# Kernel optimization log

Measured on AMD Instinct MI355X. Metric: run time of the kernel, lower is better.

## Reference

```python
import jax, jax.numpy as jnp
import numpy as np

ALPHA = 0.2  # LeakyReLU negative slope
N_NODES = 100000
N_EDGES = 3200000
IN_F = 256
OUT_F = 64

def setup_inputs() -> dict:
    key = jax.random.key(0)
    k1, k2, k3, k4 = jax.random.split(key, 4)
    inp = jax.random.uniform(k1, (N_NODES, IN_F), dtype=jnp.float32)
    edge = jax.random.randint(k2, (2, N_EDGES), 0, N_NODES, dtype=jnp.int64)
    # xavier_normal with gain=1.414
    g = 1.414
    W = jax.random.normal(k3, (IN_F, OUT_F), dtype=jnp.float32) * (g * np.sqrt(2.0 / (IN_F + OUT_F)))
    a = jax.random.normal(k4, (1, 2 * OUT_F), dtype=jnp.float32) * (g * np.sqrt(2.0 / (1 + 2 * OUT_F)))
    return {"input": inp, "edge": edge, "W": W, "a": a}

def reference(input, edge, W, a):
    N = input.shape[0]
    src, dst = edge[0], edge[1]
    h = input @ W                                  # [N, F]
    # a @ [h[src]; h[dst]] decomposed into per-node dot products
    a_src = a[0, :OUT_F]
    a_dst = a[0, OUT_F:]
    s_src = h @ a_src                              # [N]
    s_dst = h @ a_dst                              # [N]
    score = s_src[src] + s_dst[dst]                # [E]
    edge_e = jnp.exp(-jax.nn.leaky_relu(score, negative_slope=ALPHA))
    # e_rowsum = spmm(edge, edge_e, ones(N,1)) -> segment sum of edge_e over src rows
    e_rowsum = jax.ops.segment_sum(edge_e, src, num_segments=N)        # [N]
    # h_prime = spmm(edge, edge_e, h): row i = sum_e edge_e * h[dst]
    h_prime = jax.ops.segment_sum(edge_e[:, None] * h[dst], src, num_segments=N)  # [N, F]
    h_prime = h_prime / e_rowsum[:, None]
    return jax.nn.elu(h_prime)  # concat=True
```

## Files before the change

kernel.cpp:

```cpp
#include <hip/hip_runtime.h>
#include <hip/hip_bf16.h>
#include <math.h>

#define N_NODES 100000
#define N_EDGES 3200000
#define IN_F 256
#define OUT_F 64
#define LRELU_SLOPE 0.2f

#define NB 1563
#define CAP 3072

#define NBLK2 784
#define EPB 4096
#define XG 98
#define NE (NBLK2 * NB)
#define NS1 ((NE + 255) / 256)
#define S2PER ((NS1 + 255) / 256)

typedef __attribute__((ext_vector_type(8))) short bf16x8;
typedef __attribute__((ext_vector_type(4))) float f32x4;

__global__ __launch_bounds__(256) void wt_kernel(
    const float* __restrict__ W, __hip_bfloat16* __restrict__ wt) {
  wt[blockIdx.x * 256 + threadIdx.x] =
      __float2bfloat16(W[threadIdx.x * 64 + blockIdx.x]);
}

__global__ __launch_bounds__(256) void gemm_h_kernel(
    const float* __restrict__ in, const __hip_bfloat16* __restrict__ wt,
    const float* __restrict__ a, __hip_bfloat16* __restrict__ h,
    float* __restrict__ s_src, float* __restrict__ s_dst) {
  const int tid = threadIdx.x;
  const int w = tid >> 6, lane = tid & 63;
  const int lm = lane & 15, lg = lane >> 4;
  const int arow = blockIdx.x * 64 + w * 16 + lm;
  const bool rv = arow < N_NODES;
  const float* xrow = &in[(size_t)(rv ? arow : 0) * IN_F + lg * 8];

  f32x4 acc[4];
#pragma unroll
  for (int ct = 0; ct < 4; ++ct) acc[ct] = (f32x4){0.f, 0.f, 0.f, 0.f};

  const __hip_bfloat16* wbase = &wt[(size_t)lm * IN_F + lg * 8];

#pragma unroll
  for (int kt = 0; kt < 8; ++kt) {
    float4 xa = make_float4(0.f, 0.f, 0.f, 0.f);
    float4 xb = make_float4(0.f, 0.f, 0.f, 0.f);
    if (rv) {
      xa = *(const float4*)(xrow + kt * 32);
      xb = *(const float4*)(xrow + kt * 32 + 4);
    }
    union { __hip_bfloat16 s[8]; bf16x8 v; } u;
    u.s[0] = __float2bfloat16(xa.x); u.s[1] = __float2bfloat16(xa.y);
    u.s[2] = __float2bfloat16(xa.z); u.s[3] = __float2bfloat16(xa.w);
    u.s[4] = __float2bfloat16(xb.x); u.s[5] = __float2bfloat16(xb.y);
    u.s[6] = __float2bfloat16(xb.z); u.s[7] = __float2bfloat16(xb.w);
    const bf16x8 af = u.v;
#pragma unroll
    for (int ct = 0; ct < 4; ++ct) {
      bf16x8 bfr = *(const bf16x8*)(wbase + (size_t)ct * 16 * IN_F + kt * 32);
      acc[ct] = __builtin_amdgcn_mfma_f32_16x16x32_bf16(af, bfr, acc[ct],
                                                        0, 0, 0);
    }
  }

  float as[4], ad[4];
#pragma unroll
  for (int ct = 0; ct < 4; ++ct) {
    as[ct] = a[ct * 16 + lm];
    ad[ct] = a[OUT_F + ct * 16 + lm];
  }
#pragma unroll
  for (int reg = 0; reg < 4; ++reg) {
    const int row = blockIdx.x * 64 + w * 16 + lg * 4 + reg;
    float vs = 0.f, vd = 0.f;
    if (row < N_NODES) {
#pragma unroll
      for (int ct = 0; ct < 4; ++ct) {
        const float v = acc[ct][reg];
        h[(size_t)row * OUT_F + ct * 16 + lm] = __float2bfloat16(v);
        vs += v * as[ct];
        vd += v * ad[ct];
      }
    }
#pragma unroll
    for (int m = 1; m < 16; m <<= 1) {
      vs += __shfl_xor(vs, m);
      vd += __shfl_xor(vd, m);
    }
    if (lm == 0 && row < N_NODES) {
      s_src[row] = vs;
      s_dst[row] = vd;
    }
  }
}

__global__ __launch_bounds__(256) void hist2d_kernel(
    const int4* __restrict__ src4, int* __restrict__ cnt2d) {
  __shared__ int lh[NB];
  const int tid = threadIdx.x, b = blockIdx.x;
  for (int j = tid; j < NB; j += 256) lh[j] = 0;
  __syncthreads();
#pragma unroll
  for (int i = 0; i < 4; ++i) {
    const int idx4 = b * (EPB / 4) + i * 256 + tid;
    if (idx4 < N_EDGES / 4) {
      const int4 s = src4[idx4];
      atomicAdd(&lh[s.x >> 6], 1);
      atomicAdd(&lh[s.y >> 6], 1);
      atomicAdd(&lh[s.z >> 6], 1);
      atomicAdd(&lh[s.w >> 6], 1);
    }
  }
  __syncthreads();
  for (int j = tid; j < NB; j += 256) cnt2d[b * NB + j] = lh[j];
}

__device__ __forceinline__ int cnt2d_addr(int o) {
  const int j = o / NBLK2;
  const int rk = o - j * NBLK2;
  const int r = rk / XG;
  const int q = rk - r * XG;
  return (q * 8 + r) * NB + j;
}

__global__ __launch_bounds__(256) void scan1_kernel(
    int* __restrict__ cnt2d, int* __restrict__ pt) {
  __shared__ int ws[4];
  const int tid = threadIdx.x, lane = tid & 63, wv = tid >> 6;
  const int o = blockIdx.x * 256 + tid;
  int addr = 0, v = 0;
  if (o < NE) { addr = cnt2d_addr(o); v = cnt2d[addr]; }
  int incl = v;
#pragma unroll
  for (int off = 1; off < 64; off <<= 1) {
    const int t = __shfl_up(incl, off);
    if (lane >= off) incl += t;
  }
  if (lane == 63) ws[wv] = incl;
  __syncthreads();
  int base = 0;
#pragma unroll
  for (int k = 0; k < 4; ++k)
    if (k < wv) base += ws[k];
  if (o < NE) cnt2d[addr] = base + incl - v;
  if (tid == 255) pt[blockIdx.x] = base + incl;
}

__global__ __launch_bounds__(256) void scan2_kernel(int* __restrict__ pt) {
  __shared__ int ts[256];
  const int t = threadIdx.x;
  int local[S2PER];
  int sum = 0;
#pragma unroll
  for (int k = 0; k < S2PER; ++k) {
    const int o = t * S2PER + k;
    const int v = (o < NS1) ? pt[o] : 0;
    local[k] = sum;
    sum += v;
  }
  ts[t] = sum;
  __syncthreads();
  for (int off = 1; off < 256; off <<= 1) {
    int tv = (t >= off) ? ts[t - off] : 0;
    __syncthreads();
    ts[t] += tv;
    __syncthreads();
  }
  const int ex = (t > 0) ? ts[t - 1] : 0;
#pragma unroll
  for (int k = 0; k < S2PER; ++k) {
    const int o = t * S2PER + k;
    if (o < NS1) pt[o] = ex + local[k];
  }
}

__global__ __launch_bounds__(256) void scan3_kernel(
    int* __restrict__ cnt2d, const int* __restrict__ pt,
    int* __restrict__ bstart) {
  const int o = blockIdx.x * 256 + threadIdx.x;
  if (o < NE) {
    const int addr = cnt2d_addr(o);
    const int excl = cnt2d[addr] + pt[blockIdx.x];
    cnt2d[addr] = excl;
    const int j = o / NBLK2;
    if (o - j * NBLK2 == 0) bstart[j] = excl;
  }
  if (o == 0) bstart[NB] = N_EDGES;
}

__global__ __launch_bounds__(256) void scatter2_kernel(
    const int4* __restrict__ src4, const int4* __restrict__ dst4,
    const int* __restrict__ cnt2d, unsigned int* __restrict__ staged) {
  __shared__ int base[NB];
  const int tid = threadIdx.x, b = blockIdx.x;
  for (int j = tid; j < NB; j += 256) base[j] = cnt2d[b * NB + j];
  __syncthreads();
#pragma unroll
  for (int i = 0; i < 4; ++i) {
    const int idx4 = b * (EPB / 4) + i * 256 + tid;
    if (idx4 < N_EDGES / 4) {
      const int4 s = src4[idx4];
      const int4 d = dst4[idx4];
      int p;
      p = atomicAdd(&base[s.x >> 6], 1);
      staged[p] = ((unsigned)(s.x & 63) << 17) | (unsigned)d.x;
      p = atomicAdd(&base[s.y >> 6], 1);
      staged[p] = ((unsigned)(s.y & 63) << 17) | (unsigned)d.y;
      p = atomicAdd(&base[s.z >> 6], 1);
      staged[p] = ((unsigned)(s.z & 63) << 17) | (unsigned)d.z;
      p = atomicAdd(&base[s.w >> 6], 1);
      staged[p] = ((unsigned)(s.w & 63) << 17) | (unsigned)d.w;
    }
  }
}

__global__ __launch_bounds__(256) void sort_aggregate_kernel(
    const int* __restrict__ bstart, const unsigned int* __restrict__ staged,
    const float* __restrict__ s_src, const float* __restrict__ s_dst,
    const __hip_bfloat16* __restrict__ h, float* __restrict__ out) {
  __shared__ uint2 eds[CAP];
  __shared__ float ssrc[64];
  __shared__ int lcnt[64];
  __shared__ int lstart[65];
  __shared__ int lcur[64];

  const int b = blockIdx.x;
  const int tid = threadIdx.x;
  const int lane = tid & 63;
  const int wv = tid >> 6;
  const int node0 = b << 6;

  if (tid < 64)
    ssrc[tid] = (node0 + tid < N_NODES) ? s_src[node0 + tid] : 0.f;

  const int e0 = bstart[b];
  const int e1 = bstart[b + 1];

  float acc[16], rsn[16];
#pragma unroll
  for (int j = 0; j < 16; ++j) { acc[j] = 0.f; rsn[j] = 0.f; }

  for (int c0 = e0; c0 < e1; c0 += CAP) {
    const int cc = min(CAP, e1 - c0);
    __syncthreads();
    if (tid < 64) lcnt[tid] = 0;
    __syncthreads();

    for (int i = tid; i < cc; i += 256)
      atomicAdd(&lcnt[staged[c0 + i] >> 17], 1);
    __syncthreads();

    if (tid < 64) {
      int v = lcnt[tid];
#pragma unroll
      for (int off = 1; off < 64; off <<= 1) {
        int tv = __shfl_up(v, off);
        if (lane >= off) v += tv;
      }
      lstart[tid + 1] = v;
      if (tid == 0) lstart[0] = 0;
      lcur[tid] = v - lcnt[tid];
    }
    __syncthreads();

    for (int i = tid; i < cc; i += 256) {
      const unsigned pk = staged[c0 + i];
      const int ls = (int)(pk >> 17);
      const int d = (int)(pk & 0x1FFFFu);
      const float sc = ssrc[ls] + s_dst[d];
      const float lr = sc > 0.f ? sc : LRELU_SLOPE * sc;
      const float ev = __expf(-lr);
      const int p = atomicAdd(&lcur[ls], 1);
      eds[p] = make_uint2((unsigned)d, __float_as_uint(ev));
    }
    __syncthreads();

#pragma unroll
    for (int j = 0; j < 16; ++j) {
      const int n = wv + 4 * j;
      const int iend = lstart[n + 1];
      int i = lstart[n];
      float p0 = 0.f, p1 = 0.f, rv = 0.f;
      for (; i + 4 <= iend; i += 4) {
        const uint2 q0 = eds[i + 0], q1 = eds[i + 1];
        const uint2 q2 = eds[i + 2], q3 = eds[i + 3];
        const float v0 = __uint_as_float(q0.y), v1 = __uint_as_float(q1.y);
        const float v2 = __uint_as_float(q2.y), v3 = __uint_as_float(q3.y);
        const float h0 = __bfloat162float(h[(size_t)q0.x * OUT_F + lane]);
        const float h1 = __bfloat162float(h[(size_t)q1.x * OUT_F + lane]);
        const float h2 = __bfloat162float(h[(size_t)q2.x * OUT_F + lane]);
        const float h3 = __bfloat162float(h[(size_t)q3.x * OUT_F + lane]);
        p0 += v0 * h0 + v2 * h2;
        p1 += v1 * h1 + v3 * h3;
        rv += (v0 + v1) + (v2 + v3);
      }
      for (; i < iend; ++i) {
        const uint2 q0 = eds[i];
        const float v0 = __uint_as_float(q0.y);
        p0 += v0 * __bfloat162float(h[(size_t)q0.x * OUT_F + lane]);
        rv += v0;
      }
      acc[j] += p0 + p1;
      rsn[j] += rv;
    }
  }

#pragma unroll
  for (int j = 0; j < 16; ++j) {
    const int node = node0 + wv + 4 * j;
    if (node < N_NODES) {
      const float v = acc[j] / rsn[j];
      out[(size_t)node * OUT_F + lane] = v > 0.f ? v : expm1f(v);
    }
  }
}

extern "C" void kernel_launch(void* const* d_in, const int* in_sizes, int n_in,
                              void* d_out, int out_size, void* d_ws, size_t ws_size,
                              hipStream_t stream) {
  const float* in = (const float*)d_in[0];
  const int* edge = (const int*)d_in[1];
  const float* W = (const float*)d_in[2];
  const float* a = (const float*)d_in[3];
  float* out = (float*)d_out;

  const int4* src4 = (const int4*)edge;
  const int4* dst4 = (const int4*)(edge + N_EDGES);

  char* p = (char*)d_ws;
  __hip_bfloat16* h = (__hip_bfloat16*)p;  p += (size_t)N_NODES * OUT_F * 2;
  float* s_src = (float*)p;                p += (size_t)N_NODES * 4;
  float* s_dst = (float*)p;                p += (size_t)N_NODES * 4;
  unsigned int* staged = (unsigned int*)p; p += (size_t)N_EDGES * 4;
  int* bctr = (int*)p;                     p += (size_t)(NB * 32) * 4;
  int* bstart = (int*)p;                   p += (size_t)(NB + 1) * 4 + 12;
  __hip_bfloat16* wt = (__hip_bfloat16*)p; p += (size_t)OUT_F * IN_F * 2;
  (void)bctr;

  int* cnt2d = (int*)d_out;
  int* pt = (int*)((char*)d_out + (size_t)8 * 1024 * 1024);

  wt_kernel<<<OUT_F, 256, 0, stream>>>(W, wt);
  gemm_h_kernel<<<(N_NODES + 63) / 64, 256, 0, stream>>>(in, wt, a, h, s_src,
                                                         s_dst);
  hist2d_kernel<<<NBLK2, 256, 0, stream>>>(src4, cnt2d);
  scan1_kernel<<<NS1, 256, 0, stream>>>(cnt2d, pt);
  scan2_kernel<<<1, 256, 0, stream>>>(pt);
  scan3_kernel<<<NS1, 256, 0, stream>>>(cnt2d, pt, bstart);
  scatter2_kernel<<<NBLK2, 256, 0, stream>>>(src4, dst4, cnt2d, staged);
  sort_aggregate_kernel<<<NB, 256, 0, stream>>>(bstart, staged, s_src, s_dst,
                                                h, out);
}
```

Before: 416.5 us.

## Reduce bucket-sort partition blocks and use bucket-major count layout for scans

Shrinks the histogram/scatter grid from 784 to 256 blocks of 512 threads, so each block covers a larger edge chunk. The per-block count matrix becomes bucket-major with a block rank interleaved across XCD groups, so the scan reads and writes contiguously and each scan block maps exactly to one bucket. That removes the index arithmetic in the scans and lets the second-level scan write bucket starts directly. The count matrix shrinks, which cuts scan traffic, but fewer blocks means less parallelism in the atomic-heavy histogram and scatter passes.

```diff
diff --git a/kernel.cpp b/kernel.cpp
--- a/kernel.cpp
+++ b/kernel.cpp
@@ -11,12 +11,11 @@
 #define NB 1563
 #define CAP 3072
 
-#define NBLK2 784
-#define EPB 4096
-#define XG 98
-#define NE (NBLK2 * NB)
-#define NS1 ((NE + 255) / 256)
-#define S2PER ((NS1 + 255) / 256)
+#define NBLK2 256
+#define XG 32
+#define I4PB (N_EDGES / 4 / NBLK2)
+#define NE (NB * NBLK2)
+#define S2PER ((NB + 255) / 256)
 
 typedef __attribute__((ext_vector_type(8))) short bf16x8;
 typedef __attribute__((ext_vector_type(4))) float f32x4;
@@ -97,17 +96,19 @@
   }
 }
 
-__global__ __launch_bounds__(256) void hist2d_kernel(
+__global__ __launch_bounds__(512) void hist2d_kernel(
     const int4* __restrict__ src4, int* __restrict__ cnt2d) {
   __shared__ int lh[NB];
   const int tid = threadIdx.x, b = blockIdx.x;
-  for (int j = tid; j < NB; j += 256) lh[j] = 0;
-  __syncthreads();
-#pragma unroll
-  for (int i = 0; i < 4; ++i) {
-    const int idx4 = b * (EPB / 4) + i * 256 + tid;
-    if (idx4 < N_EDGES / 4) {
-      const int4 s = src4[idx4];
+  const int rank = (b & 7) * XG + (b >> 3);
+  for (int j = tid; j < NB; j += 512) lh[j] = 0;
+  __syncthreads();
+  const int base4 = b * I4PB;
+#pragma unroll
+  for (int i = 0; i < 7; ++i) {
+    const int k = i * 512 + tid;
+    if (k < I4PB) {
+      const int4 s = src4[base4 + k];
       atomicAdd(&lh[s.x >> 6], 1);
       atomicAdd(&lh[s.y >> 6], 1);
       atomicAdd(&lh[s.z >> 6], 1);
@@ -115,15 +116,7 @@
     }
   }
   __syncthreads();
-  for (int j = tid; j < NB; j += 256) cnt2d[b * NB + j] = lh[j];
-}
-
-__device__ __forceinline__ int cnt2d_addr(int o) {
-  const int j = o / NBLK2;
-  const int rk = o - j * NBLK2;
-  const int r = rk / XG;
-  const int q = rk - r * XG;
-  return (q * 8 + r) * NB + j;
+  for (int j = tid; j < NB; j += 512) cnt2d[j * NBLK2 + rank] = lh[j];
 }
 
 __global__ __launch_bounds__(256) void scan1_kernel(
@@ -131,8 +124,7 @@
   __shared__ int ws[4];
   const int tid = threadIdx.x, lane = tid & 63, wv = tid >> 6;
   const int o = blockIdx.x * 256 + tid;
-  int addr = 0, v = 0;
-  if (o < NE) { addr = cnt2d_addr(o); v = cnt2d[addr]; }
+  const int v = cnt2d[o];
   int incl = v;
 #pragma unroll
   for (int off = 1; off < 64; off <<= 1) {
@@ -145,11 +137,12 @@
 #pragma unroll
   for (int k = 0; k < 4; ++k)
     if (k < wv) base += ws[k];
-  if (o < NE) cnt2d[addr] = base + incl - v;
+  cnt2d[o] = base + incl - v;
   if (tid == 255) pt[blockIdx.x] = base + incl;
 }
 
-__global__ __launch_bounds__(256) void scan2_kernel(int* __restrict__ pt) {
+__global__ __launch_bounds__(256) void scan2_kernel(
+    int* __restrict__ pt, int* __restrict__ bstart) {
   __shared__ int ts[256];
   const int t = threadIdx.x;
   int local[S2PER];
@@ -157,7 +150,7 @@
 #pragma unroll
   for (int k = 0; k < S2PER; ++k) {
     const int o = t * S2PER + k;
-    const int v = (o < NS1) ? pt[o] : 0;
+    const int v = (o < NB) ? pt[o] : 0;
     local[k] = sum;
     sum += v;
   }
@@ -173,37 +166,35 @@
 #pragma unroll
   for (int k = 0; k < S2PER; ++k) {
     const int o = t * S2PER + k;
-    if (o < NS1) pt[o] = ex + local[k];
-  }
+    if (o < NB) {
+      pt[o] = ex + local[k];
+      bstart[o] = ex + local[k];
+    }
+  }
+  if (t == 0) bstart[NB] = N_EDGES;
 }
 
 __global__ __launch_bounds__(256) void scan3_kernel(
-    int* __restrict__ cnt2d, const int* __restrict__ pt,
-    int* __restrict__ bstart) {
+    int* __restrict__ cnt2d, const int* __restrict__ pt) {
   const int o = blockIdx.x * 256 + threadIdx.x;
-  if (o < NE) {
-    const int addr = cnt2d_addr(o);
-    const int excl = cnt2d[addr] + pt[blockIdx.x];
-    cnt2d[addr] = excl;
-    const int j = o / NBLK2;
-    if (o - j * NBLK2 == 0) bstart[j] = excl;
-  }
-  if (o == 0) bstart[NB] = N_EDGES;
-}
-
-__global__ __launch_bounds__(256) void scatter2_kernel(
+  cnt2d[o] += pt[blockIdx.x];
+}
+
+__global__ __launch_bounds__(512) void scatter2_kernel(
     const int4* __restrict__ src4, const int4* __restrict__ dst4,
     const int* __restrict__ cnt2d, unsigned int* __restrict__ staged) {
   __shared__ int base[NB];
   const int tid = threadIdx.x, b = blockIdx.x;
-  for (int j = tid; j < NB; j += 256) base[j] = cnt2d[b * NB + j];
-  __syncthreads();
-#pragma unroll
-  for (int i = 0; i < 4; ++i) {
-    const int idx4 = b * (EPB / 4) + i * 256 + tid;
-    if (idx4 < N_EDGES / 4) {
-      const int4 s = src4[idx4];
-      const int4 d = dst4[idx4];
+  const int rank = (b & 7) * XG + (b >> 3);
+  for (int j = tid; j < NB; j += 512) base[j] = cnt2d[j * NBLK2 + rank];
+  __syncthreads();
+  const int base4 = b * I4PB;
+#pragma unroll
+  for (int i = 0; i < 7; ++i) {
+    const int k = i * 512 + tid;
+    if (k < I4PB) {
+      const int4 s = src4[base4 + k];
+      const int4 d = dst4[base4 + k];
       int p;
       p = atomicAdd(&base[s.x >> 6], 1);
       staged[p] = ((unsigned)(s.x & 63) << 17) | (unsigned)d.x;
@@ -346,11 +337,11 @@
   wt_kernel<<<OUT_F, 256, 0, stream>>>(W, wt);
   gemm_h_kernel<<<(N_NODES + 63) / 64, 256, 0, stream>>>(in, wt, a, h, s_src,
                                                          s_dst);
-  hist2d_kernel<<<NBLK2, 256, 0, stream>>>(src4, cnt2d);
-  scan1_kernel<<<NS1, 256, 0, stream>>>(cnt2d, pt);
-  scan2_kernel<<<1, 256, 0, stream>>>(pt);
-  scan3_kernel<<<NS1, 256, 0, stream>>>(cnt2d, pt, bstart);
-  scatter2_kernel<<<NBLK2, 256, 0, stream>>>(src4, dst4, cnt2d, staged);
+  hist2d_kernel<<<NBLK2, 512, 0, stream>>>(src4, cnt2d);
+  scan1_kernel<<<NB, 256, 0, stream>>>(cnt2d, pt);
+  scan2_kernel<<<1, 256, 0, stream>>>(pt, bstart);
+  scan3_kernel<<<NB, 256, 0, stream>>>(cnt2d, pt);
+  scatter2_kernel<<<NBLK2, 512, 0, stream>>>(src4, dst4, cnt2d, staged);
   sort_aggregate_kernel<<<NB, 256, 0, stream>>>(bstart, staged, s_src, s_dst,
                                                 h, out);
 }
```

Result: faster. 382.9 us (-8.1%).
